# Kernel tuning notes

Measured on AMD Instinct MI355X. Metric: run time of the kernel, lower is better.

## Reference

```python
import jax, jax.numpy as jnp
import numpy as np

V = 50000      # num variables (= num pos literals = num neg literals)
L = 2 * V      # num literals
C = 210000     # num clauses
E = 315000     # edges per polarity
H = 128        # hidden size
R = 4          # message-passing rounds


def _unif(k, shape, s):
    return jax.random.uniform(k, shape, jnp.float32, -s, s)


def setup_inputs() -> dict:
    key = jax.random.key(0)
    ks = jax.random.split(key, 40)
    d = {}
    d["l_embedding"] = jax.random.normal(ks[0], (L, H), jnp.float32)
    d["c_embedding"] = jax.random.normal(ks[1], (C, H), jnp.float32)
    d["edge_pos_src"] = jax.random.randint(ks[2], (E,), 0, V)
    d["edge_pos_dst"] = jax.random.randint(ks[3], (E,), 0, C)
    d["edge_neg_src"] = jax.random.randint(ks[4], (E,), 0, V)
    d["edge_neg_dst"] = jax.random.randint(ks[5], (E,), 0, C)
    s = 1.0 / np.sqrt(H)
    i = 6
    # 3-layer MLPs (Linear->ReLU->Linear->ReLU->Linear), weights stored [in, out]
    for pre in ("lmlp", "cmlp"):
        for j in range(3):
            d[f"{pre}_w{j}"] = _unif(ks[i], (H, H), s); i += 1
            d[f"{pre}_b{j}"] = _unif(ks[i], (H,), s); i += 1
    # LSTM cells: gate order i,f,g,o packed along last dim (4H)
    d["l_w_ih"] = _unif(ks[i], (2 * H, 4 * H), s); i += 1
    d["l_w_hh"] = _unif(ks[i], (H, 4 * H), s); i += 1
    d["l_b"] = _unif(ks[i], (4 * H,), s); i += 1   # b_ih + b_hh fused
    d["c_w_ih"] = _unif(ks[i], (H, 4 * H), s); i += 1
    d["c_w_hh"] = _unif(ks[i], (H, 4 * H), s); i += 1
    d["c_b"] = _unif(ks[i], (4 * H,), s); i += 1
    return d


def _mlp3(x, w0, b0, w1, b1, w2, b2):
    x = jax.nn.relu(x @ w0 + b0)
    x = jax.nn.relu(x @ w1 + b1)
    return x @ w2 + b2


def _lstm_cell(x, h, c, w_ih, w_hh, b):
    g = x @ w_ih + h @ w_hh + b          # [N, 4H]
    gi, gf, gg, go = jnp.split(g, 4, axis=-1)
    c_new = jax.nn.sigmoid(gf) * c + jax.nn.sigmoid(gi) * jnp.tanh(gg)
    h_new = jax.nn.sigmoid(go) * jnp.tanh(c_new)
    return h_new, c_new


def reference(l_embedding, c_embedding, edge_pos_src, edge_pos_dst,
              edge_neg_src, edge_neg_dst,
              lmlp_w0, lmlp_b0, lmlp_w1, lmlp_b1, lmlp_w2, lmlp_b2,
              cmlp_w0, cmlp_b0, cmlp_w1, cmlp_b1, cmlp_w2, cmlp_b2,
              l_w_ih, l_w_hh, l_b, c_w_ih, c_w_hh, c_b):
    seg = jax.ops.segment_sum
    l_h, l_c = l_embedding, jnp.zeros_like(l_embedding)
    c_h, c_c = c_embedding, jnp.zeros_like(c_embedding)
    for _ in range(R):
        # literal -> clause messages
        l_msg = _mlp3(l_h, lmlp_w0, lmlp_b0, lmlp_w1, lmlp_b1, lmlp_w2, lmlp_b2)
        pos_msg, neg_msg = jnp.split(l_msg, 2, axis=0)  # [V,H] each
        l2c = (seg(pos_msg[edge_pos_src], edge_pos_dst, num_segments=C)
               + seg(neg_msg[edge_neg_src], edge_neg_dst, num_segments=C))
        # clause -> literal messages
        c_msg = _mlp3(c_h, cmlp_w0, cmlp_b0, cmlp_w1, cmlp_b1, cmlp_w2, cmlp_b2)
        pos_c2l = seg(c_msg[edge_pos_dst], edge_pos_src, num_segments=V)
        neg_c2l = seg(c_msg[edge_neg_dst], edge_neg_src, num_segments=V)
        c2l = jnp.concatenate([pos_c2l, neg_c2l], axis=0)  # [2V,H]
        # flip literal hidden (pos <-> neg halves)
        flip = jnp.concatenate([l_h[V:], l_h[:V]], axis=0)
        # LSTM updates (seq_len=1 torch LSTM == one cell step)
        c_h, c_c = _lstm_cell(l2c, c_h, c_c, c_w_ih, c_w_hh, c_b)
        l_h, l_c = _lstm_cell(jnp.concatenate([c2l, flip], axis=1),
                              l_h, l_c, l_w_ih, l_w_hh, l_b)
    return (l_h, c_h)
```

## Files before the change

kernel.cpp:

```cpp
#include <hip/hip_runtime.h>
#include <hip/hip_bf16.h>

#define HDIM 128

using u16 = unsigned short;
using u32 = unsigned int;
using bf16x8 = __attribute__((ext_vector_type(8))) short;
using f32x4  = __attribute__((ext_vector_type(4))) float;

__device__ __forceinline__ float bf2f(u32 b) {
  union { u32 i; float f; } x; x.i = b << 16; return x.f;
}
__device__ __forceinline__ u16 f2bf(float f) {
  union { float f; u32 i; } x; x.f = f; u32 u = x.i;
  return (u16)((u + 0x7fffu + ((u >> 16) & 1u)) >> 16);
}
__device__ __forceinline__ void unpack8(uint4 r, float* o) {
  o[0] = bf2f(r.x & 0xffffu); o[1] = bf2f(r.x >> 16);
  o[2] = bf2f(r.y & 0xffffu); o[3] = bf2f(r.y >> 16);
  o[4] = bf2f(r.z & 0xffffu); o[5] = bf2f(r.z >> 16);
  o[6] = bf2f(r.w & 0xffffu); o[7] = bf2f(r.w >> 16);
}
__device__ __forceinline__ float sigm_f(float x) {
  return __builtin_amdgcn_rcpf(1.f + __expf(-x));
}
__device__ __forceinline__ float tanh_f(float x) {
  return 2.f * __builtin_amdgcn_rcpf(1.f + __expf(-2.f * x)) - 1.f;
}

__global__ __launch_bounds__(256) void k_detect(const u32* __restrict__ probe,
                                                int* __restrict__ flag) {
  __shared__ int cnt;
  if (threadIdx.x == 0) cnt = 0;
  __syncthreads();
  int local = 0;
  for (int i = threadIdx.x; i < 1024; i += 256) {
    u32 e = (probe[i] >> 7) & 0xFF;
    if (e >= 96 && e <= 126) local++;
  }
  atomicAdd(&cnt, local);
  __syncthreads();
  if (threadIdx.x == 0) *flag = (cnt > 512) ? 1 : 0;
}

__global__ __launch_bounds__(256) void k_any_to_f32(
    const void* __restrict__ src, float* __restrict__ dst, int n8,
    const int* __restrict__ flag) {
  int i = blockIdx.x * 256 + threadIdx.x;
  if (i >= n8) return;
  float t[8];
  if (*flag) {
    uint4 raw = ((const uint4*)src)[i];
    unpack8(raw, t);
  } else {
    const float4* s = ((const float4*)src) + 2 * (size_t)i;
    float4 a = s[0], b = s[1];
    t[0] = a.x; t[1] = a.y; t[2] = a.z; t[3] = a.w;
    t[4] = b.x; t[5] = b.y; t[6] = b.z; t[7] = b.w;
  }
  float4* o = ((float4*)dst) + 2 * (size_t)i;
  o[0] = make_float4(t[0], t[1], t[2], t[3]);
  o[1] = make_float4(t[4], t[5], t[6], t[7]);
}

__global__ __launch_bounds__(256) void k_any_to_bf16(
    const void* __restrict__ src, u16* __restrict__ dst, int n8,
    const int* __restrict__ flag) {
  int i = blockIdx.x * 256 + threadIdx.x;
  if (i >= n8) return;
  uint4 o;
  if (*flag) {
    o = ((const uint4*)src)[i];
  } else {
    const float4* s = ((const float4*)src) + 2 * (size_t)i;
    float4 a = s[0], b = s[1];
    o.x = (u32)f2bf(a.x) | ((u32)f2bf(a.y) << 16);
    o.y = (u32)f2bf(a.z) | ((u32)f2bf(a.w) << 16);
    o.z = (u32)f2bf(b.x) | ((u32)f2bf(b.y) << 16);
    o.w = (u32)f2bf(b.z) | ((u32)f2bf(b.w) << 16);
  }
  ((uint4*)dst)[i] = o;
}

__global__ __launch_bounds__(256) void k_build_wt(
    const void* __restrict__ Wih, const void* __restrict__ Whh, int KX, int Ktot,
    int Ncols, u16* __restrict__ WT, const int* __restrict__ flag) {
  int idx = blockIdx.x * 256 + threadIdx.x;
  int total = Ncols * Ktot;
  if (idx >= total) return;
  int n = idx / Ktot, k = idx - n * Ktot;
  const void* src = (k < KX) ? Wih : Whh;
  int kk = (k < KX) ? k : k - KX;
  size_t off = (size_t)kk * Ncols + n;
  u16 b;
  if (*flag) b = ((const u16*)src)[off];
  else       b = f2bf(((const float*)src)[off]);
  WT[(size_t)n * Ktot + k] = b;
}

__global__ __launch_bounds__(256) void k_sentinel(float* __restrict__ out,
                                                  int n, float val) {
  int i = blockIdx.x * 256 + threadIdx.x;
  if (i < n) out[i] = val;
}

__global__ __launch_bounds__(256) void k_count(
    const int* __restrict__ key, int key_add, int E, int* __restrict__ deg) {
  int e = blockIdx.x * 256 + threadIdx.x;
  if (e < E) atomicAdd(&deg[key[e] + key_add], 1);
}

__global__ __launch_bounds__(256) void k_scan1(
    const int* __restrict__ in, int* __restrict__ inc,
    int* __restrict__ bsum, int n) {
  __shared__ int s[256];
  const int tid = threadIdx.x;
  const int b0 = blockIdx.x * 1024;
  int v[4]; int sum = 0;
#pragma unroll
  for (int j = 0; j < 4; ++j) {
    int i = b0 + tid * 4 + j;
    int x = (i < n) ? in[i] : 0;
    sum += x; v[j] = sum;
  }
  s[tid] = sum;
  __syncthreads();
  for (int d = 1; d < 256; d <<= 1) {
    int t = (tid >= d) ? s[tid - d] : 0;
    __syncthreads();
    s[tid] += t;
    __syncthreads();
  }
  int base = (tid > 0) ? s[tid - 1] : 0;
#pragma unroll
  for (int j = 0; j < 4; ++j) {
    int i = b0 + tid * 4 + j;
    if (i < n) inc[i] = base + v[j];
  }
  if (tid == 255) bsum[blockIdx.x] = s[255];
}

__global__ __launch_bounds__(256) void k_scan2(int* __restrict__ bsum, int nb) {
  __shared__ int s[256];
  const int tid = threadIdx.x;
  int x = (tid < nb) ? bsum[tid] : 0;
  s[tid] = x;
  __syncthreads();
  for (int d = 1; d < 256; d <<= 1) {
    int t = (tid >= d) ? s[tid - d] : 0;
    __syncthreads();
    s[tid] += t;
    __syncthreads();
  }
  if (tid < nb) bsum[tid] = (tid > 0) ? s[tid - 1] : 0;
}

__global__ __launch_bounds__(256) void k_scan3(
    const int* __restrict__ inc, const int* __restrict__ bsum,
    int* __restrict__ off, int* __restrict__ cursor, int n) {
  int i = blockIdx.x * 256 + threadIdx.x;
  if (i < n) {
    int v = inc[i] + bsum[i >> 10];
    off[i + 1] = v;
    int prev = (i & 1023) ? (inc[i - 1] + bsum[i >> 10]) : bsum[i >> 10];
    cursor[i] = prev;
    if (i == 0) { off[0] = 0; cursor[0] = 0; }
  }
}

__global__ __launch_bounds__(256) void k_fill(
    const int* __restrict__ key, int key_add,
    const int* __restrict__ pay, int pay_add, int E,
    int* __restrict__ cursor, int* __restrict__ vals) {
  int e = blockIdx.x * 256 + threadIdx.x;
  if (e >= E) return;
  int k = key[e] + key_add;
  int p = atomicAdd(&cursor[k], 1);
  vals[p] = pay[e] + pay_add;
}

__global__ __launch_bounds__(256) void k_mlp3(
    const u16* __restrict__ X, u16* __restrict__ Y, int N,
    const u16* __restrict__ WT0, const float* __restrict__ B0,
    const u16* __restrict__ WT1, const float* __restrict__ B1,
    const u16* __restrict__ WT2, const float* __restrict__ B2) {
  __shared__ u16 xs[128 * 128];
  const int tid = threadIdx.x;
  const int lane = tid & 63;
  const int w = tid >> 6;
  const int lr = lane & 15;
  const int hi = lane >> 4;
  const int lk = hi * 8;
  const int row0 = blockIdx.x * 128;

  {
    const int row = tid >> 1, half = tid & 1;
    const int grow = row0 + row;
#pragma unroll
    for (int j = 0; j < 8; ++j) {
      int g = half * 8 + j;
      uint4 v = {0, 0, 0, 0};
      if (grow < N) v = *reinterpret_cast<const uint4*>(X + (size_t)grow * HDIM + g * 8);
      ((uint4*)xs)[row * 16 + (g ^ (row & 7))] = v;
    }
  }
  __syncthreads();

  const u16* WTs[3] = {WT0, WT1, WT2};
  const float* Bs[3] = {B0, B1, B2};
#pragma unroll
  for (int layer = 0; layer < 3; ++layer) {
    f32x4 zc = {0.f, 0.f, 0.f, 0.f};
    f32x4 acc[8][2];
#pragma unroll
    for (int rt = 0; rt < 8; ++rt) { acc[rt][0] = zc; acc[rt][1] = zc; }
#pragma unroll
    for (int ks = 0; ks < 4; ++ks) {
      bf16x8 bfr[2];
#pragma unroll
      for (int t = 0; t < 2; ++t) {
        int col = w * 32 + t * 16 + lr;
        bfr[t] = *reinterpret_cast<const bf16x8*>(
            WTs[layer] + (size_t)col * HDIM + ks * 32 + lk);
      }
#pragma unroll
      for (int rt = 0; rt < 8; ++rt) {
        int row = rt * 16 + lr;
        int g = ks * 4 + hi;
        bf16x8 a = ((const bf16x8*)xs)[row * 16 + (g ^ (row & 7))];
        acc[rt][0] = __builtin_amdgcn_mfma_f32_16x16x32_bf16(a, bfr[0], acc[rt][0], 0, 0, 0);
        acc[rt][1] = __builtin_amdgcn_mfma_f32_16x16x32_bf16(a, bfr[1], acc[rt][1], 0, 0, 0);
      }
    }
    float bv[2];
    bv[0] = Bs[layer][w * 32 + lr];
    bv[1] = Bs[layer][w * 32 + 16 + lr];
    __syncthreads();
    if (layer < 2) {
#pragma unroll
      for (int rt = 0; rt < 8; ++rt)
#pragma unroll
        for (int t = 0; t < 2; ++t) {
          int col = w * 32 + t * 16 + lr;
          int g = col >> 3, cw = col & 7;
#pragma unroll
          for (int reg = 0; reg < 4; ++reg) {
            int row = rt * 16 + hi * 4 + reg;
            float v = fmaxf(acc[rt][t][reg] + bv[t], 0.f);
            xs[(row * 16 + (g ^ (row & 7))) * 8 + cw] = f2bf(v);
          }
        }
      __syncthreads();
    } else {
#pragma unroll
      for (int rt = 0; rt < 8; ++rt)
#pragma unroll
        for (int t = 0; t < 2; ++t) {
          int col = w * 32 + t * 16 + lr;
#pragma unroll
          for (int reg = 0; reg < 4; ++reg) {
            int row = row0 + rt * 16 + hi * 4 + reg;
            if (row < N) Y[(size_t)row * HDIM + col] = f2bf(acc[rt][t][reg] + bv[t]);
          }
        }
    }
  }
}

template<int HAS_X1, int OUT_F32>
__global__ __launch_bounds__(512) void k_lstm3(
    const u16* __restrict__ msgs, const int* __restrict__ moff,
    const int* __restrict__ mvals,
    const u16* __restrict__ X1, int Vhalf,
    const u16* __restrict__ Hin, const float* __restrict__ Cin,
    void* __restrict__ Hout, float* __restrict__ Cout,
    const u16* __restrict__ WT, const float* __restrict__ Bias, int N) {
  const int KT = HAS_X1 ? 384 : 256;
  const int KS = KT / 32;
  const int G = KT / 8;
  __shared__ u16 xs[64 * (HAS_X1 ? 384 : 256)];
  const int tid = threadIdx.x;
  const int lane = tid & 63;
  const int w = tid >> 6;
  const int lr = lane & 15;
  const int hi = lane >> 4;
  const int lk = hi * 8;
  const int row0 = blockIdx.x * 64;

  {
    const int row = tid >> 3, sub = tid & 7;
    const int grow = row0 + row;
    const int swz = row & 7;
    uint4* lds = (uint4*)xs + row * G;
    float a[16];
#pragma unroll
    for (int t = 0; t < 16; ++t) a[t] = 0.f;
    if (grow < N) {
      int s0 = moff[grow], s1 = moff[grow + 1];
      for (int j = s0; j < s1; ++j) {
        const uint4* p = reinterpret_cast<const uint4*>(
            msgs + (size_t)mvals[j] * HDIM + sub * 16);
        uint4 r0 = p[0], r1 = p[1];
        float f0[8], f1[8];
        unpack8(r0, f0); unpack8(r1, f1);
#pragma unroll
        for (int t = 0; t < 8; ++t) { a[t] += f0[t]; a[8 + t] += f1[t]; }
      }
    }
    uint4 pk;
    pk.x = (u32)f2bf(a[0]) | ((u32)f2bf(a[1]) << 16);
    pk.y = (u32)f2bf(a[2]) | ((u32)f2bf(a[3]) << 16);
    pk.z = (u32)f2bf(a[4]) | ((u32)f2bf(a[5]) << 16);
    pk.w = (u32)f2bf(a[6]) | ((u32)f2bf(a[7]) << 16);
    lds[(sub * 2) ^ swz] = pk;
    pk.x = (u32)f2bf(a[8])  | ((u32)f2bf(a[9])  << 16);
    pk.y = (u32)f2bf(a[10]) | ((u32)f2bf(a[11]) << 16);
    pk.z = (u32)f2bf(a[12]) | ((u32)f2bf(a[13]) << 16);
    pk.w = (u32)f2bf(a[14]) | ((u32)f2bf(a[15]) << 16);
    lds[(sub * 2 + 1) ^ swz] = pk;
    if (HAS_X1) {
      uint4 v0 = {0, 0, 0, 0}, v1 = {0, 0, 0, 0};
      if (grow < N) {
        int sr = (grow < Vhalf) ? grow + Vhalf : grow - Vhalf;
        const uint4* p = reinterpret_cast<const uint4*>(X1 + (size_t)sr * HDIM + sub * 16);
        v0 = p[0]; v1 = p[1];
      }
      lds[(16 + sub * 2) ^ swz] = v0;
      lds[(16 + sub * 2 + 1) ^ swz] = v1;
    }
    {
      uint4 v0 = {0, 0, 0, 0}, v1 = {0, 0, 0, 0};
      if (grow < N) {
        const uint4* p = reinterpret_cast<const uint4*>(Hin + (size_t)grow * HDIM + sub * 16);
        v0 = p[0]; v1 = p[1];
      }
      int gb = (HAS_X1 ? 32 : 16) + sub * 2;
      lds[gb ^ swz] = v0;
      lds[(gb + 1) ^ swz] = v1;
    }
  }
  __syncthreads();

  f32x4 zc = {0.f, 0.f, 0.f, 0.f};
  f32x4 acc[4][4];
#pragma unroll
  for (int rt = 0; rt < 4; ++rt)
#pragma unroll
    for (int q = 0; q < 4; ++q) acc[rt][q] = zc;

#pragma unroll
  for (int ks = 0; ks < KS; ++ks) {
    bf16x8 bfr[4];
#pragma unroll
    for (int q = 0; q < 4; ++q) {
      int col = q * 128 + w * 16 + lr;
      bfr[q] = *reinterpret_cast<const bf16x8*>(WT + (size_t)col * KT + ks * 32 + lk);
    }
#pragma unroll
    for (int rt = 0; rt < 4; ++rt) {
      int row = rt * 16 + lr;
      bf16x8 a = ((const bf16x8*)xs)[row * G + ((ks * 4 + hi) ^ (row & 7))];
#pragma unroll
      for (int q = 0; q < 4; ++q)
        acc[rt][q] = __builtin_amdgcn_mfma_f32_16x16x32_bf16(a, bfr[q], acc[rt][q], 0, 0, 0);
    }
  }

  const int m = w * 16 + lr;
  float bv[4];
#pragma unroll
  for (int q = 0; q < 4; ++q) bv[q] = Bias[q * 128 + m];

  if (row0 + 64 <= N) {
#pragma unroll
    for (int rt = 0; rt < 4; ++rt) {
      size_t cb = ((size_t)((row0 >> 4) + rt) * 128 + m) * 16 + hi * 4;
      float4 cin = *reinterpret_cast<const float4*>(Cin + cb);
      float4 cout;
      float hn[4];
#pragma unroll
      for (int reg = 0; reg < 4; ++reg) {
        float gi = acc[rt][0][reg] + bv[0];
        float gf = acc[rt][1][reg] + bv[1];
        float gg = acc[rt][2][reg] + bv[2];
        float go = acc[rt][3][reg] + bv[3];
        float co = (&cin.x)[reg];
        float cn = sigm_f(gf) * co + sigm_f(gi) * tanh_f(gg);
        hn[reg] = sigm_f(go) * tanh_f(cn);
        (&cout.x)[reg] = cn;
      }
      *reinterpret_cast<float4*>(Cout + cb) = cout;
      int rowb = row0 + rt * 16 + hi * 4;
#pragma unroll
      for (int reg = 0; reg < 4; ++reg) {
        size_t hidx = (size_t)(rowb + reg) * HDIM + m;
        if (OUT_F32) ((float*)Hout)[hidx] = hn[reg];
        else         ((u16*)Hout)[hidx]   = f2bf(hn[reg]);
      }
    }
  } else {
#pragma unroll
    for (int rt = 0; rt < 4; ++rt)
#pragma unroll
      for (int reg = 0; reg < 4; ++reg) {
        int row = row0 + rt * 16 + hi * 4 + reg;
        if (row >= N) continue;
        size_t cb = ((size_t)(row >> 4) * 128 + m) * 16 + (row & 15);
        float gi = acc[rt][0][reg] + bv[0];
        float gf = acc[rt][1][reg] + bv[1];
        float gg = acc[rt][2][reg] + bv[2];
        float go = acc[rt][3][reg] + bv[3];
        float co = Cin[cb];
        float cn = sigm_f(gf) * co + sigm_f(gi) * tanh_f(gg);
        float hn = sigm_f(go) * tanh_f(cn);
        Cout[cb] = cn;
        size_t hidx = (size_t)row * HDIM + m;
        if (OUT_F32) ((float*)Hout)[hidx] = hn;
        else         ((u16*)Hout)[hidx]   = f2bf(hn);
      }
  }
}

extern "C" void kernel_launch(void* const* d_in, const int* in_sizes, int n_in,
                              void* d_out, int out_size, void* d_ws, size_t ws_size,
                              hipStream_t stream) {
  const int V = in_sizes[0] / (2 * HDIM);
  const int L = 2 * V;
  const int C = in_sizes[1] / HDIM;
  const int E = in_sizes[2];
  const int R = 4;

  const void* l_emb = d_in[0];
  const void* c_emb = d_in[1];
  const int* eps  = (const int*)d_in[2];
  const int* epd  = (const int*)d_in[3];
  const int* ens  = (const int*)d_in[4];
  const int* end_ = (const int*)d_in[5];

  const size_t LH = (size_t)L * HDIM;
  const size_t CH = (size_t)C * HDIM;

  char* base = (char*)d_ws;
  auto alloc = [&](size_t bytes) -> char* {
    char* r = base; base += (bytes + 255) / 256 * 256; return r;
  };
  u16* l_hA  = (u16*)alloc(LH * 2);
  u16* l_hB  = (u16*)alloc(LH * 2);
  u16* c_h   = (u16*)alloc(CH * 2);
  u16* tL    = (u16*)alloc(LH * 2);
  u16* tC    = (u16*)alloc(CH * 2);
  float* l_c = (float*)alloc(LH * 4);
  float* c_c = (float*)alloc(CH * 4);
  u16* WT_lmlp[3]; u16* WT_cmlp[3];
  for (int j = 0; j < 3; ++j) WT_lmlp[j] = (u16*)alloc(HDIM * HDIM * 2);
  for (int j = 0; j < 3; ++j) WT_cmlp[j] = (u16*)alloc(HDIM * HDIM * 2);
  u16* WT_l = (u16*)alloc(512 * 384 * 2);
  u16* WT_c = (u16*)alloc(512 * 256 * 2);
  float* Bf_lmlp[3]; float* Bf_cmlp[3];
  for (int j = 0; j < 3; ++j) Bf_lmlp[j] = (float*)alloc(HDIM * 4);
  for (int j = 0; j < 3; ++j) Bf_cmlp[j] = (float*)alloc(HDIM * 4);
  float* Bf_l = (float*)alloc(512 * 4);
  float* Bf_c = (float*)alloc(512 * 4);
  int* deg1 = (int*)alloc((size_t)C * 4);
  int* off1 = (int*)alloc(((size_t)C + 1) * 4);
  int* cur1 = (int*)alloc((size_t)C * 4);
  int* vals1 = (int*)alloc((size_t)2 * E * 4);
  int* deg2 = (int*)alloc((size_t)L * 4);
  int* off2 = (int*)alloc(((size_t)L + 1) * 4);
  int* cur2 = (int*)alloc((size_t)L * 4);
  int* vals2 = (int*)alloc((size_t)2 * E * 4);
  int* inc  = (int*)alloc((size_t)(C > L ? C : L) * 4);
  int* bsum = (int*)alloc(256 * 4);
  int* flag = (int*)alloc(256);

  size_t required = (size_t)(base - (char*)d_ws);
  if (required > ws_size) {
    float val = 64.0f + (float)(ws_size >> 26);
    k_sentinel<<<(out_size + 255) / 256, 256, 0, stream>>>((float*)d_out, out_size, val);
    return;
  }

  k_detect<<<1, 256, 0, stream>>>((const u32*)d_in[6], flag);
  const int mlp_tot = HDIM * HDIM;
  for (int j = 0; j < 3; ++j) {
    k_build_wt<<<(mlp_tot + 255) / 256, 256, 0, stream>>>(
        d_in[6 + 2 * j], d_in[6 + 2 * j], HDIM, HDIM, HDIM, WT_lmlp[j], flag);
    k_build_wt<<<(mlp_tot + 255) / 256, 256, 0, stream>>>(
        d_in[12 + 2 * j], d_in[12 + 2 * j], HDIM, HDIM, HDIM, WT_cmlp[j], flag);
  }
  k_build_wt<<<(512 * 384 + 255) / 256, 256, 0, stream>>>(
      d_in[18], d_in[19], 256, 384, 512, WT_l, flag);
  k_build_wt<<<(512 * 256 + 255) / 256, 256, 0, stream>>>(
      d_in[21], d_in[22], 128, 256, 512, WT_c, flag);
  k_any_to_f32<<<1, 256, 0, stream>>>(d_in[7],  Bf_lmlp[0], HDIM / 8, flag);
  k_any_to_f32<<<1, 256, 0, stream>>>(d_in[9],  Bf_lmlp[1], HDIM / 8, flag);
  k_any_to_f32<<<1, 256, 0, stream>>>(d_in[11], Bf_lmlp[2], HDIM / 8, flag);
  k_any_to_f32<<<1, 256, 0, stream>>>(d_in[13], Bf_cmlp[0], HDIM / 8, flag);
  k_any_to_f32<<<1, 256, 0, stream>>>(d_in[15], Bf_cmlp[1], HDIM / 8, flag);
  k_any_to_f32<<<1, 256, 0, stream>>>(d_in[17], Bf_cmlp[2], HDIM / 8, flag);
  k_any_to_f32<<<1, 256, 0, stream>>>(d_in[20], Bf_l, 512 / 8, flag);
  k_any_to_f32<<<1, 256, 0, stream>>>(d_in[23], Bf_c, 512 / 8, flag);

  const int gE = (E + 255) / 256;
  (void)hipMemsetAsync(deg1, 0, (size_t)C * 4, stream);
  (void)hipMemsetAsync(deg2, 0, (size_t)L * 4, stream);
  k_count<<<gE, 256, 0, stream>>>(epd, 0, E, deg1);
  k_count<<<gE, 256, 0, stream>>>(end_, 0, E, deg1);
  k_count<<<gE, 256, 0, stream>>>(eps, 0, E, deg2);
  k_count<<<gE, 256, 0, stream>>>(ens, V, E, deg2);
  {
    int nb = (C + 1023) / 1024;
    k_scan1<<<nb, 256, 0, stream>>>(deg1, inc, bsum, C);
    k_scan2<<<1, 256, 0, stream>>>(bsum, nb);
    k_scan3<<<(C + 255) / 256, 256, 0, stream>>>(inc, bsum, off1, cur1, C);
  }
  {
    int nb = (L + 1023) / 1024;
    k_scan1<<<nb, 256, 0, stream>>>(deg2, inc, bsum, L);
    k_scan2<<<1, 256, 0, stream>>>(bsum, nb);
    k_scan3<<<(L + 255) / 256, 256, 0, stream>>>(inc, bsum, off2, cur2, L);
  }
  k_fill<<<gE, 256, 0, stream>>>(epd, 0, eps, 0, E, cur1, vals1);
  k_fill<<<gE, 256, 0, stream>>>(end_, 0, ens, V, E, cur1, vals1);
  k_fill<<<gE, 256, 0, stream>>>(eps, 0, epd, 0, E, cur2, vals2);
  k_fill<<<gE, 256, 0, stream>>>(ens, V, end_, 0, E, cur2, vals2);

  k_any_to_bf16<<<(int)((LH / 8 + 255) / 256), 256, 0, stream>>>(l_emb, l_hA, (int)(LH / 8), flag);
  k_any_to_bf16<<<(int)((CH / 8 + 255) / 256), 256, 0, stream>>>(c_emb, c_h, (int)(CH / 8), flag);
  (void)hipMemsetAsync(l_c, 0, LH * sizeof(float), stream);
  (void)hipMemsetAsync(c_c, 0, CH * sizeof(float), stream);

  u16* lh_cur = l_hA;
  u16* lh_nxt = l_hB;
  float* outf = (float*)d_out;

  const int gm_l = (L + 127) / 128;
  const int gm_c = (C + 127) / 128;
  const int gs_c = (C + 63) / 64;
  const int gs_l = (L + 63) / 64;

  for (int r = 0; r < R; ++r) {
    k_mlp3<<<gm_l, 256, 0, stream>>>(lh_cur, tL, L,
        WT_lmlp[0], Bf_lmlp[0], WT_lmlp[1], Bf_lmlp[1], WT_lmlp[2], Bf_lmlp[2]);
    k_mlp3<<<gm_c, 256, 0, stream>>>(c_h, tC, C,
        WT_cmlp[0], Bf_cmlp[0], WT_cmlp[1], Bf_cmlp[1], WT_cmlp[2], Bf_cmlp[2]);
    if (r == R - 1) {
      k_lstm3<0, 1><<<gs_c, 512, 0, stream>>>(
          tL, off1, vals1, (const u16*)nullptr, 0, c_h, c_c,
          (void*)(outf + LH), c_c, WT_c, Bf_c, C);
      k_lstm3<1, 1><<<gs_l, 512, 0, stream>>>(
          tC, off2, vals2, lh_cur, V, lh_cur, l_c,
          (void*)outf, l_c, WT_l, Bf_l, L);
    } else {
      k_lstm3<0, 0><<<gs_c, 512, 0, stream>>>(
          tL, off1, vals1, (const u16*)nullptr, 0, c_h, c_c,
          (void*)c_h, c_c, WT_c, Bf_c, C);
      k_lstm3<1, 0><<<gs_l, 512, 0, stream>>>(
          tC, off2, vals2, lh_cur, V, lh_cur, l_c,
          (void*)lh_nxt, l_c, WT_l, Bf_l, L);
      u16* tmp = lh_cur; lh_cur = lh_nxt; lh_nxt = tmp;
    }
  }
}
```

Before: 2.166 ms.

## Merge literal and clause MLP/LSTM launches into dual kernels; widen gather lanes

Each round's two MLP launches become one launch whose blocks branch on block id to the literal or clause work, and the same is done for the two LSTM launches. This cuts launch count and lets the smaller and larger grids share the GPU at once instead of draining one after the other. The LSTM gather is also reorganised so 16 threads cover a row with one 16-byte load each over two row passes, doubling gather parallelism per row and issuing the Hin and flip loads before the message loop. The dual LSTM kernel uses the larger 384-column LDS buffer for both paths and sets a min-blocks hint of 8, which may limit occupancy or raise register pressure.

```diff
diff --git a/kernel.cpp b/kernel.cpp
--- a/kernel.cpp
+++ b/kernel.cpp
@@ -179,19 +179,17 @@
   vals[p] = pay[e] + pay_add;
 }
 
-__global__ __launch_bounds__(256) void k_mlp3(
+__device__ __forceinline__ void mlp3_body(
+    u16* xs, int tid, int row0,
     const u16* __restrict__ X, u16* __restrict__ Y, int N,
     const u16* __restrict__ WT0, const float* __restrict__ B0,
     const u16* __restrict__ WT1, const float* __restrict__ B1,
     const u16* __restrict__ WT2, const float* __restrict__ B2) {
-  __shared__ u16 xs[128 * 128];
-  const int tid = threadIdx.x;
   const int lane = tid & 63;
   const int w = tid >> 6;
   const int lr = lane & 15;
   const int hi = lane >> 4;
   const int lk = hi * 8;
-  const int row0 = blockIdx.x * 128;
 
   {
     const int row = tid >> 1, half = tid & 1;
@@ -267,8 +265,26 @@
   }
 }
 
+__global__ __launch_bounds__(256) void k_mlp3_dual(
+    const u16* __restrict__ Xl, u16* __restrict__ Yl, int NL, int nblkL,
+    const u16* __restrict__ WL0, const float* __restrict__ BL0,
+    const u16* __restrict__ WL1, const float* __restrict__ BL1,
+    const u16* __restrict__ WL2, const float* __restrict__ BL2,
+    const u16* __restrict__ Xc, u16* __restrict__ Yc, int NC,
+    const u16* __restrict__ WC0, const float* __restrict__ BC0,
+    const u16* __restrict__ WC1, const float* __restrict__ BC1,
+    const u16* __restrict__ WC2, const float* __restrict__ BC2) {
+  __shared__ u16 xs[128 * 128];
+  int bid = blockIdx.x;
+  if (bid < nblkL)
+    mlp3_body(xs, threadIdx.x, bid * 128, Xl, Yl, NL, WL0, BL0, WL1, BL1, WL2, BL2);
+  else
+    mlp3_body(xs, threadIdx.x, (bid - nblkL) * 128, Xc, Yc, NC, WC0, BC0, WC1, BC1, WC2, BC2);
+}
+
 template<int HAS_X1, int OUT_F32>
-__global__ __launch_bounds__(512) void k_lstm3(
+__device__ __forceinline__ void lstm_body(
+    u16* xs, int tid, int row0,
     const u16* __restrict__ msgs, const int* __restrict__ moff,
     const int* __restrict__ mvals,
     const u16* __restrict__ X1, int Vhalf,
@@ -278,33 +294,38 @@
   const int KT = HAS_X1 ? 384 : 256;
   const int KS = KT / 32;
   const int G = KT / 8;
-  __shared__ u16 xs[64 * (HAS_X1 ? 384 : 256)];
-  const int tid = threadIdx.x;
   const int lane = tid & 63;
   const int w = tid >> 6;
   const int lr = lane & 15;
   const int hi = lane >> 4;
   const int lk = hi * 8;
-  const int row0 = blockIdx.x * 64;
-
-  {
-    const int row = tid >> 3, sub = tid & 7;
+
+#pragma unroll
+  for (int p = 0; p < 2; ++p) {
+    const int row = (tid >> 4) + p * 32;
+    const int sub = tid & 15;
     const int grow = row0 + row;
     const int swz = row & 7;
     uint4* lds = (uint4*)xs + row * G;
-    float a[16];
-#pragma unroll
-    for (int t = 0; t < 16; ++t) a[t] = 0.f;
+    uint4 vh = {0, 0, 0, 0}, vx = {0, 0, 0, 0};
+    if (grow < N) {
+      vh = *reinterpret_cast<const uint4*>(Hin + (size_t)grow * HDIM + sub * 8);
+      if (HAS_X1) {
+        int sr = (grow < Vhalf) ? grow + Vhalf : grow - Vhalf;
+        vx = *reinterpret_cast<const uint4*>(X1 + (size_t)sr * HDIM + sub * 8);
+      }
+    }
+    float a[8];
+#pragma unroll
+    for (int t = 0; t < 8; ++t) a[t] = 0.f;
     if (grow < N) {
       int s0 = moff[grow], s1 = moff[grow + 1];
       for (int j = s0; j < s1; ++j) {
-        const uint4* p = reinterpret_cast<const uint4*>(
-            msgs + (size_t)mvals[j] * HDIM + sub * 16);
-        uint4 r0 = p[0], r1 = p[1];
-        float f0[8], f1[8];
-        unpack8(r0, f0); unpack8(r1, f1);
-#pragma unroll
-        for (int t = 0; t < 8; ++t) { a[t] += f0[t]; a[8 + t] += f1[t]; }
+        uint4 r = *reinterpret_cast<const uint4*>(
+            msgs + (size_t)mvals[j] * HDIM + sub * 8);
+        float f[8]; unpack8(r, f);
+#pragma unroll
+        for (int t = 0; t < 8; ++t) a[t] += f[t];
       }
     }
     uint4 pk;
@@ -312,32 +333,9 @@
     pk.y = (u32)f2bf(a[2]) | ((u32)f2bf(a[3]) << 16);
     pk.z = (u32)f2bf(a[4]) | ((u32)f2bf(a[5]) << 16);
     pk.w = (u32)f2bf(a[6]) | ((u32)f2bf(a[7]) << 16);
-    lds[(sub * 2) ^ swz] = pk;
-    pk.x = (u32)f2bf(a[8])  | ((u32)f2bf(a[9])  << 16);
-    pk.y = (u32)f2bf(a[10]) | ((u32)f2bf(a[11]) << 16);
-    pk.z = (u32)f2bf(a[12]) | ((u32)f2bf(a[13]) << 16);
-    pk.w = (u32)f2bf(a[14]) | ((u32)f2bf(a[15]) << 16);
-    lds[(sub * 2 + 1) ^ swz] = pk;
-    if (HAS_X1) {
-      uint4 v0 = {0, 0, 0, 0}, v1 = {0, 0, 0, 0};
-      if (grow < N) {
-        int sr = (grow < Vhalf) ? grow + Vhalf : grow - Vhalf;
-        const uint4* p = reinterpret_cast<const uint4*>(X1 + (size_t)sr * HDIM + sub * 16);
-        v0 = p[0]; v1 = p[1];
-      }
-      lds[(16 + sub * 2) ^ swz] = v0;
-      lds[(16 + sub * 2 + 1) ^ swz] = v1;
-    }
-    {
-      uint4 v0 = {0, 0, 0, 0}, v1 = {0, 0, 0, 0};
-      if (grow < N) {
-        const uint4* p = reinterpret_cast<const uint4*>(Hin + (size_t)grow * HDIM + sub * 16);
-        v0 = p[0]; v1 = p[1];
-      }
-      int gb = (HAS_X1 ? 32 : 16) + sub * 2;
-      lds[gb ^ swz] = v0;
-      lds[(gb + 1) ^ swz] = v1;
-    }
+    lds[sub ^ swz] = pk;
+    if (HAS_X1) lds[(16 + sub) ^ swz] = vx;
+    lds[((HAS_X1 ? 32 : 16) + sub) ^ swz] = vh;
   }
   __syncthreads();
 
@@ -419,6 +417,29 @@
         else         ((u16*)Hout)[hidx]   = f2bf(hn);
       }
   }
+}
+
+template<int OUT_F32>
+__global__ __launch_bounds__(512, 8) void k_lstm_dual(
+    const u16* __restrict__ msgsL, const int* __restrict__ offL,
+    const int* __restrict__ valsL,
+    const u16* __restrict__ X1L, int Vhalf,
+    const u16* __restrict__ HinL, const float* __restrict__ CinL,
+    void* __restrict__ HoutL, float* __restrict__ CoutL,
+    const u16* __restrict__ WTl, const float* __restrict__ Bl, int NL, int nblkL,
+    const u16* __restrict__ msgsC, const int* __restrict__ offC,
+    const int* __restrict__ valsC,
+    const u16* __restrict__ HinC, const float* __restrict__ CinC,
+    void* __restrict__ HoutC, float* __restrict__ CoutC,
+    const u16* __restrict__ WTc, const float* __restrict__ Bc, int NC) {
+  __shared__ u16 xs[64 * 384];
+  int bid = blockIdx.x;
+  if (bid < nblkL)
+    lstm_body<1, OUT_F32>(xs, threadIdx.x, bid * 64, msgsL, offL, valsL,
+                          X1L, Vhalf, HinL, CinL, HoutL, CoutL, WTl, Bl, NL);
+  else
+    lstm_body<0, OUT_F32>(xs, threadIdx.x, (bid - nblkL) * 64, msgsC, offC, valsC,
+                          (const u16*)nullptr, 0, HinC, CinC, HoutC, CoutC, WTc, Bc, NC);
 }
 
 extern "C" void kernel_launch(void* const* d_in, const int* in_sizes, int n_in,
@@ -540,24 +561,23 @@
   const int gs_l = (L + 63) / 64;
 
   for (int r = 0; r < R; ++r) {
-    k_mlp3<<<gm_l, 256, 0, stream>>>(lh_cur, tL, L,
-        WT_lmlp[0], Bf_lmlp[0], WT_lmlp[1], Bf_lmlp[1], WT_lmlp[2], Bf_lmlp[2]);
-    k_mlp3<<<gm_c, 256, 0, stream>>>(c_h, tC, C,
+    k_mlp3_dual<<<gm_l + gm_c, 256, 0, stream>>>(
+        lh_cur, tL, L, gm_l,
+        WT_lmlp[0], Bf_lmlp[0], WT_lmlp[1], Bf_lmlp[1], WT_lmlp[2], Bf_lmlp[2],
+        c_h, tC, C,
         WT_cmlp[0], Bf_cmlp[0], WT_cmlp[1], Bf_cmlp[1], WT_cmlp[2], Bf_cmlp[2]);
     if (r == R - 1) {
-      k_lstm3<0, 1><<<gs_c, 512, 0, stream>>>(
-          tL, off1, vals1, (const u16*)nullptr, 0, c_h, c_c,
-          (void*)(outf + LH), c_c, WT_c, Bf_c, C);
-      k_lstm3<1, 1><<<gs_l, 512, 0, stream>>>(
-          tC, off2, vals2, lh_cur, V, lh_cur, l_c,
-          (void*)outf, l_c, WT_l, Bf_l, L);
+      k_lstm_dual<1><<<gs_l + gs_c, 512, 0, stream>>>(
+          tC, off2, vals2, lh_cur, V, lh_cur, l_c, (void*)outf, l_c,
+          WT_l, Bf_l, L, gs_l,
+          tL, off1, vals1, c_h, c_c, (void*)(outf + LH), c_c,
+          WT_c, Bf_c, C);
     } else {
-      k_lstm3<0, 0><<<gs_c, 512, 0, stream>>>(
-          tL, off1, vals1, (const u16*)nullptr, 0, c_h, c_c,
-          (void*)c_h, c_c, WT_c, Bf_c, C);
-      k_lstm3<1, 0><<<gs_l, 512, 0, stream>>>(
-          tC, off2, vals2, lh_cur, V, lh_cur, l_c,
-          (void*)lh_nxt, l_c, WT_l, Bf_l, L);
+      k_lstm_dual<0><<<gs_l + gs_c, 512, 0, stream>>>(
+          tC, off2, vals2, lh_cur, V, lh_cur, l_c, (void*)lh_nxt, l_c,
+          WT_l, Bf_l, L, gs_l,
+          tL, off1, vals1, c_h, c_c, (void*)c_h, c_c,
+          WT_c, Bf_c, C);
       u16* tmp = lh_cur; lh_cur = lh_nxt; lh_nxt = tmp;
     }
   }
```

New measurement: 2.397 ms. 1.11x slower.
